# Kernel optimization log

Measured on AMD Instinct MI355X. Metric: run time of the kernel, lower is better.

## Reference

```python
import jax, jax.numpy as jnp
import numpy as np
from jax import lax

N_FFT = 1024
N_FREQ = N_FFT // 2 + 1  # 513
BATCH = 32
SAMPLES = 480000
HOP = 256


def setup_inputs() -> dict:
    key = jax.random.key(0)
    kx, kwin = jax.random.split(key)
    x = jax.random.normal(kx, (BATCH, 1, SAMPLES), dtype=jnp.float32)
    n = jnp.arange(N_FFT, dtype=jnp.float32)
    # standard rfft angular frequencies: w_k = 2*pi*k / N
    w = 2.0 * jnp.pi * jnp.arange(N_FREQ, dtype=jnp.float32) / N_FFT
    # Hann window (periodic), as typically used for STFT
    window = 0.5 - 0.5 * jnp.cos(2.0 * jnp.pi * jnp.arange(N_FFT, dtype=jnp.float32) / N_FFT)
    return {"x": x, "n": n, "w": w, "window": window, "hop_size": HOP, "power": 1}


def _create_dft_matrices(n, w, window):
    # temp[f, t] = w_f * n_t
    temp = w[:, None] * n[None, :]              # [n_freq, n_fft]
    Fr = jnp.cos(temp)
    Fi = -jnp.sin(temp)
    if window is not None:
        Fr = window * Fr
        Fi = window * Fi
    # conv1d weights: [out_ch=n_freq, in_ch=1, kernel=n_fft]
    return Fr[:, None, :], Fi[:, None, :]


def reference(x, n, w, window, hop_size, power):
    DFTr, DFTi = _create_dft_matrices(n, w, window)
    dn = ("NCH", "OIH", "NCH")
    real_x = lax.conv_general_dilated(x, DFTr, (hop_size,), "VALID", dimension_numbers=dn)
    imag_x = lax.conv_general_dilated(x, DFTi, (hop_size,), "VALID", dimension_numbers=dn)
    S = real_x ** 2 + imag_x ** 2              # [B, n_freq, n_frames]
    if not power:
        S = jnp.sqrt(S)
    return S
```

## Files before the change

kernel.cpp:

```cpp
#include <hip/hip_runtime.h>
#include <hip/hip_bf16.h>
#include <stdint.h>
#include <math.h>


#define NFFT     1024
#define NFREQ    513
#define BATCH    32
#define SAMPLES  480000
#define SAMPH    240000
#define HOPH     128
#define NFRAMES  1872
#define BN       128
#define NBPB     15
#define MBLKS    4
#define KTILES   16
#define NWG      (BATCH * NBPB * MBLKS)

#define XH_BYTES  ((size_t)BATCH * SAMPLES)
#define AWS_BYTES ((size_t)MBLKS * KTILES * 128 * 64)
#define TW_BYTES  (513 * 8)

#define XMAX   6.5f
#define SCALE_X (127.0f / XMAX)
#define DEQ    (XMAX / 16129.0f)
#define DEQ2   (DEQ * DEQ)

#define QX_BLOCKS 1875
#define BA_BLOCKS 2048
#define PREP_BLOCKS (QX_BLOCKS + BA_BLOCKS + 1)

typedef __attribute__((ext_vector_type(4)))  int i32x4;
typedef __attribute__((ext_vector_type(16))) int i32x16;

#define SLOTM(r) ((((r) >> 1) & 3) ^ (((r) >> 3) & 1))
#define SWZ(q) ((q) ^ ((((q) >> 3) ^ ((q) >> 6)) & 7))

__global__ __launch_bounds__(256) void k_prep(const float* __restrict__ x,
                                              const float* __restrict__ narr,
                                              const float* __restrict__ w,
                                              const float* __restrict__ window,
                                              signed char* __restrict__ xe,
                                              signed char* __restrict__ xo,
                                              signed char* __restrict__ Aws,
                                              float2* __restrict__ tw) {
  const int bid = blockIdx.x;
  const int tid = threadIdx.x;
  if (bid < QX_BLOCKS) {
    size_t i = (size_t)bid * 256 + tid;
    const float4* x4 = (const float4*)x;
    union { signed char c[16]; uint4 v; } pe, po;
    #pragma unroll
    for (int j = 0; j < 8; ++j) {
      float4 a = x4[i * 8 + j];
      float qe  = fminf(127.f, fmaxf(-127.f, a.x * SCALE_X));
      float qo  = fminf(127.f, fmaxf(-127.f, a.y * SCALE_X));
      float qe2 = fminf(127.f, fmaxf(-127.f, a.z * SCALE_X));
      float qo2 = fminf(127.f, fmaxf(-127.f, a.w * SCALE_X));
      pe.c[j * 2]     = (signed char)__float2int_rn(qe);
      po.c[j * 2]     = (signed char)__float2int_rn(qo);
      pe.c[j * 2 + 1] = (signed char)__float2int_rn(qe2);
      po.c[j * 2 + 1] = (signed char)__float2int_rn(qo2);
    }
    ((uint4*)xe)[i] = pe.v;
    ((uint4*)xo)[i] = po.v;
  } else if (bid < QX_BLOCKS + BA_BLOCKS) {
    uint32_t E = (uint32_t)(bid - QX_BLOCKS) * 256 + tid;
    uint32_t e    = E & 15;
    uint32_t s    = (E >> 4) & 3;
    uint32_t r    = (E >> 6) & 127;
    uint32_t kt   = (E >> 13) & 15;
    uint32_t mblk = E >> 17;
    uint32_t er = mblk * 128 + r;
    uint32_t j  = (kt & 7) * 64 + ((s ^ SLOTM(r)) << 4) + e;
    uint32_t odd = (kt >> 3) & 1;
    uint32_t widx = (er == 1) ? 512u : (er & ~1u);
    float ang = w[widx] * narr[j];
    float sn, cs;
    sincosf(ang, &sn, &cs);
    float base = ((er & 1) && (er != 1)) ? -sn : cs;
    float val = 127.f * window[2 * j + odd] * base;
    Aws[E] = (signed char)__float2int_rn(val);
  } else {
    for (int j = tid; j <= 512; j += 256) {
      float st, ct;
      sincosf((float)j * (float)(M_PI / 512.0), &st, &ct);
      tw[j] = make_float2(ct, st);
    }
  }
}

#define GL2LDS(g, l) __builtin_amdgcn_global_load_lds( \
    (const __attribute__((address_space(1))) uint32_t*)(g), \
    (__attribute__((address_space(3))) uint32_t*)(l), 16, 0, 0)

#define WAITV4_BAR() asm volatile("s_waitcnt vmcnt(4)\ns_barrier" ::: "memory")
#define WAIT0_BAR()  asm volatile("s_waitcnt vmcnt(0)\ns_barrier" ::: "memory")
#define LGKM0_BAR()  asm volatile("s_waitcnt lgkmcnt(0)\ns_barrier" ::: "memory")

#define SE 0
#define SO 17408
#define AR 34816

#define STAGE_STREAM(src, bl) do {                                              \
  _Pragma("unroll") for (int p_ = 0; p_ < 4; ++p_) {                            \
    int q_ = p_ * 256 + tid;                                                    \
    GL2LDS((src) + (SWZ(q_) << 4), &lds[(bl) + q_ * 16]);                       \
  }                                                                             \
  if (tid < 64) {                                                               \
    int q_ = 1024 + tid;                                                        \
    GL2LDS((src) + (SWZ(q_) << 4), &lds[(bl) + q_ * 16]);                       \
  }                                                                             \
} while (0)

#define STAGE_A(kt) do {                                                        \
  _Pragma("unroll") for (int j_ = 0; j_ < 2; ++j_) {                            \
    int ci_ = j_ * 256 + tid;                                                   \
    GL2LDS(Aws + (((size_t)mblk * KTILES + (kt)) * 512 + ci_) * 16,             \
           &lds[AR + ((kt) & 3) * 8192 + ci_ * 16]);                            \
  } } while (0)

#define READ_A2(dst, kt)                                                        \
  _Pragma("unroll") for (int mt_ = 0; mt_ < 2; ++mt_)                           \
  _Pragma("unroll") for (int ks_ = 0; ks_ < 2; ++ks_) {                         \
    int r_ = wr * 64 + mt_ * 32 + lr;                                           \
    int sl_ = (ks_ * 2 + hi) ^ SLOTM(r_);                                       \
    dst[mt_][ks_] = *(const i32x4*)&lds[AR + ((kt) & 3) * 8192 + (r_ * 4 + sl_) * 16]; \
  }

#define READ_B2(dst, ktm7, SB)                                                  \
  _Pragma("unroll") for (int nt_ = 0; nt_ < 2; ++nt_)                           \
  _Pragma("unroll") for (int ks_ = 0; ks_ < 2; ++ks_) {                         \
    int cp_ = (wc * 64 + nt_ * 32 + lr) * 8 + (ktm7) * 4 + 2 * ks_ + hi;        \
    dst[nt_][ks_] = *(const i32x4*)&lds[(SB) + (SWZ(cp_) << 4)];                \
  }

#define MFMA8(ACC, A_, B_) do {                                                 \
  __builtin_amdgcn_s_setprio(1);                                                \
  _Pragma("unroll") for (int ks_ = 0; ks_ < 2; ++ks_)                           \
  _Pragma("unroll") for (int mt_ = 0; mt_ < 2; ++mt_)                           \
  _Pragma("unroll") for (int nt_ = 0; nt_ < 2; ++nt_)                           \
    ACC[mt_][nt_] = __builtin_amdgcn_mfma_i32_32x32x32_i8(                      \
        A_[mt_][ks_], B_[nt_][ks_], ACC[mt_][nt_], 0, 0, 0);                    \
  __builtin_amdgcn_s_setprio(0);                                                \
  } while (0)

#define ITER(i, ACC, SB) do {                                                   \
    if ((i) == 7) WAIT0_BAR(); else WAITV4_BAR();                               \
    i32x4 a0[2][2], a1[2][2], b0[2][2], b1[2][2];                               \
    READ_A2(a0, 2 * (i));     READ_B2(b0, (2 * (i)) & 7, SB);                   \
    READ_A2(a1, 2 * (i) + 1); READ_B2(b1, (2 * (i) + 1) & 7, SB);               \
    MFMA8(ACC, a0, b0);                                                         \
    MFMA8(ACC, a1, b1);                                                         \
    LGKM0_BAR();                                                                \
    if ((i) < 6) { STAGE_A(2 * (i) + 4); STAGE_A(2 * (i) + 5); }                \
  } while (0)

__global__ __launch_bounds__(256, 2) void k_stft(const signed char* __restrict__ xe,
                                                 const signed char* __restrict__ xo,
                                                 const signed char* __restrict__ Aws,
                                                 const float2* __restrict__ tw,
                                                 float* __restrict__ out) {
  __shared__ __align__(16) signed char lds[67584];
  const int tid  = threadIdx.x;
  const int lane = tid & 63;
  const int wid  = tid >> 6;
  const int wr = wid >> 1;
  const int wc = wid & 1;
  const int lr = lane & 31;
  const int hi = lane >> 5;

  const int bx = blockIdx.x;
  const int v = (bx & 7) * 240 + (bx >> 3);
  const int mblk = v & 3;
  const int nb = v >> 2;
  const int b  = nb / NBPB;
  const int f0 = (nb - b * NBPB) * BN;

  const signed char* se_src = xe + (size_t)b * SAMPH + (size_t)f0 * HOPH;
  const signed char* so_src = xo + (size_t)b * SAMPH + (size_t)f0 * HOPH;

  i32x16 accE[2][2], accO[2][2];
  #pragma unroll
  for (int i = 0; i < 2; ++i)
    #pragma unroll
    for (int j = 0; j < 2; ++j)
      #pragma unroll
      for (int e = 0; e < 16; ++e) { accE[i][j][e] = 0; accO[i][j][e] = 0; }

  STAGE_STREAM(se_src, SE);
  STAGE_STREAM(so_src, SO);
  STAGE_A(0); STAGE_A(1); STAGE_A(2); STAGE_A(3);
  WAIT0_BAR();

  ITER(0, accE, SE); ITER(1, accE, SE); ITER(2, accE, SE); ITER(3, accE, SE);
  ITER(4, accO, SO); ITER(5, accO, SO); ITER(6, accO, SO); ITER(7, accO, SO);

  const int fbase = mblk * 64 + wr * 32;
  #pragma unroll
  for (int nt = 0; nt < 2; ++nt) {
    const int col = wc * 64 + nt * 32 + lr;
    const int tfi = f0 + col;
    if (tfi >= NFRAMES) continue;
    float* op = out + (size_t)b * ((size_t)NFREQ * NFRAMES) + tfi;
    #pragma unroll
    for (int mt = 0; mt < 2; ++mt) {
      i32x16 vE = accE[mt][nt];
      i32x16 vO = accO[mt][nt];
      #pragma unroll
      for (int aa = 0; aa < 4; ++aa)
        #pragma unroll
        for (int q = 0; q < 2; ++q) {
          const int fq = fbase + mt * 16 + aa * 4 + 2 * hi + q;
          float Ere = (float)vE[aa * 4 + 2 * q];
          float Eim = (float)vE[aa * 4 + 2 * q + 1];
          float Ore = (float)vO[aa * 4 + 2 * q];
          float Oim = (float)vO[aa * 4 + 2 * q + 1];
          if (fq == 0) {
            float sp = Ere + Ore, sm = Ere - Ore;
            op[0]                     = DEQ2 * sp * sp;
            op[(size_t)512 * NFRAMES] = DEQ2 * sm * sm;
            op[(size_t)256 * NFRAMES] = DEQ2 * (Eim * Eim + Oim * Oim);
          } else {
            float2 t = tw[fq];
            float Pre = t.x * Ore + t.y * Oim;
            float Pim = t.x * Oim - t.y * Ore;
            float ar = Ere + Pre, ai = Eim + Pim;
            float br = Ere - Pre, bi = Eim - Pim;
            op[(size_t)fq * NFRAMES]         = DEQ2 * (ar * ar + ai * ai);
            op[(size_t)(512 - fq) * NFRAMES] = DEQ2 * (br * br + bi * bi);
          }
        }
    }
  }
}

extern "C" void kernel_launch(void* const* d_in, const int* in_sizes, int n_in,
                              void* d_out, int out_size, void* d_ws, size_t ws_size,
                              hipStream_t stream) {
  const float* x      = (const float*)d_in[0];
  const float* narr   = (const float*)d_in[1];
  const float* w      = (const float*)d_in[2];
  const float* window = (const float*)d_in[3];
  float* out = (float*)d_out;

  signed char* xe  = (signed char*)d_ws;
  signed char* xo  = xe + (size_t)BATCH * SAMPH;
  signed char* Aws = xo + (size_t)BATCH * SAMPH;
  float2*      tw  = (float2*)(Aws + AWS_BYTES);
  if (ws_size < XH_BYTES + AWS_BYTES + TW_BYTES) return;

  k_prep<<<PREP_BLOCKS, 256, 0, stream>>>(x, narr, w, window, xe, xo, Aws, tw);
  k_stft<<<NWG, 256, 0, stream>>>(xe, xo, Aws, tw, out);
}
```

Before: 64.47 us.

## Loop over all frequency blocks per workgroup, reusing staged signal tile

Each workgroup now handles all four frequency blocks for one batch/frame tile in a sequential loop instead of one block per workgroup. The staged even/odd signal in LDS is reused across all four blocks, which cuts redundant global-to-LDS signal loads, and the A-matrix stream is pipelined continuously across the blocks. The frame tile shrinks to 120 with 16 tiles per batch, giving 512 workgroups instead of 1920. This lowers parallelism and tail balance, and the epilogue stores are serialized inside the loop.

Result: slower. 96.38 us (+49.5%).

```diff
diff --git a/kernel.cpp b/kernel.cpp
--- a/kernel.cpp
+++ b/kernel.cpp
@@ -11,14 +11,13 @@
 #define SAMPH    240000
 #define HOPH     128
 #define NFRAMES  1872
-#define BN       128
-#define NBPB     15
-#define MBLKS    4
-#define KTILES   16
-#define NWG      (BATCH * NBPB * MBLKS)
+#define BN       120
+#define NBPB     16
+#define NTILES   64
+#define NWG      (BATCH * NBPB)
 
 #define XH_BYTES  ((size_t)BATCH * SAMPLES)
-#define AWS_BYTES ((size_t)MBLKS * KTILES * 128 * 64)
+#define AWS_BYTES ((size_t)NTILES * 128 * 64)
 #define TW_BYTES  (513 * 8)
 
 #define XMAX   6.5f
@@ -110,22 +109,21 @@
   if (tid < 64) {                                                               \
     int q_ = 1024 + tid;                                                        \
     GL2LDS((src) + (SWZ(q_) << 4), &lds[(bl) + q_ * 16]);                       \
-  }                                                                             \
-} while (0)
-
-#define STAGE_A(kt) do {                                                        \
+  } } while (0)
+
+#define STAGE_A(t) do {                                                         \
   _Pragma("unroll") for (int j_ = 0; j_ < 2; ++j_) {                            \
     int ci_ = j_ * 256 + tid;                                                   \
-    GL2LDS(Aws + (((size_t)mblk * KTILES + (kt)) * 512 + ci_) * 16,             \
-           &lds[AR + ((kt) & 3) * 8192 + ci_ * 16]);                            \
+    GL2LDS(Aws + ((size_t)(t) * 512 + ci_) * 16,                                \
+           &lds[AR + ((t) & 3) * 8192 + ci_ * 16]);                             \
   } } while (0)
 
-#define READ_A2(dst, kt)                                                        \
+#define READ_A2(dst, t)                                                         \
   _Pragma("unroll") for (int mt_ = 0; mt_ < 2; ++mt_)                           \
   _Pragma("unroll") for (int ks_ = 0; ks_ < 2; ++ks_) {                         \
     int r_ = wr * 64 + mt_ * 32 + lr;                                           \
     int sl_ = (ks_ * 2 + hi) ^ SLOTM(r_);                                       \
-    dst[mt_][ks_] = *(const i32x4*)&lds[AR + ((kt) & 3) * 8192 + (r_ * 4 + sl_) * 16]; \
+    dst[mt_][ks_] = *(const i32x4*)&lds[AR + ((t) & 3) * 8192 + (r_ * 4 + sl_) * 16]; \
   }
 
 #define READ_B2(dst, ktm7, SB)                                                  \
@@ -145,15 +143,17 @@
   __builtin_amdgcn_s_setprio(0);                                                \
   } while (0)
 
-#define ITER(i, ACC, SB) do {                                                   \
-    if ((i) == 7) WAIT0_BAR(); else WAITV4_BAR();                               \
+#define ITER(tb, ii, ACC, SB) do {                                              \
+    const int t0_ = (tb) + 2 * (ii), t1_ = t0_ + 1;                             \
+    const int gi_ = t0_ >> 1;                                                   \
+    if (gi_ == 31) WAIT0_BAR(); else WAITV4_BAR();                              \
     i32x4 a0[2][2], a1[2][2], b0[2][2], b1[2][2];                               \
-    READ_A2(a0, 2 * (i));     READ_B2(b0, (2 * (i)) & 7, SB);                   \
-    READ_A2(a1, 2 * (i) + 1); READ_B2(b1, (2 * (i) + 1) & 7, SB);               \
+    READ_A2(a0, t0_); READ_B2(b0, t0_ & 7, SB);                                 \
+    READ_A2(a1, t1_); READ_B2(b1, t1_ & 7, SB);                                 \
     MFMA8(ACC, a0, b0);                                                         \
     MFMA8(ACC, a1, b1);                                                         \
     LGKM0_BAR();                                                                \
-    if ((i) < 6) { STAGE_A(2 * (i) + 4); STAGE_A(2 * (i) + 5); }                \
+    if (gi_ < 30) { STAGE_A(t0_ + 4); STAGE_A(t1_ + 4); }                       \
   } while (0)
 
 __global__ __launch_bounds__(256, 2) void k_stft(const signed char* __restrict__ xe,
@@ -171,11 +171,9 @@
   const int hi = lane >> 5;
 
   const int bx = blockIdx.x;
-  const int v = (bx & 7) * 240 + (bx >> 3);
-  const int mblk = v & 3;
-  const int nb = v >> 2;
-  const int b  = nb / NBPB;
-  const int f0 = (nb - b * NBPB) * BN;
+  const int nb = (bx & 7) * 64 + (bx >> 3);
+  const int b  = nb >> 4;
+  const int f0 = (nb & 15) * BN;
 
   const signed char* se_src = xe + (size_t)b * SAMPH + (size_t)f0 * HOPH;
   const signed char* so_src = xo + (size_t)b * SAMPH + (size_t)f0 * HOPH;
@@ -193,45 +191,58 @@
   STAGE_A(0); STAGE_A(1); STAGE_A(2); STAGE_A(3);
   WAIT0_BAR();
 
-  ITER(0, accE, SE); ITER(1, accE, SE); ITER(2, accE, SE); ITER(3, accE, SE);
-  ITER(4, accO, SO); ITER(5, accO, SO); ITER(6, accO, SO); ITER(7, accO, SO);
-
-  const int fbase = mblk * 64 + wr * 32;
-  #pragma unroll
-  for (int nt = 0; nt < 2; ++nt) {
-    const int col = wc * 64 + nt * 32 + lr;
-    const int tfi = f0 + col;
-    if (tfi >= NFRAMES) continue;
-    float* op = out + (size_t)b * ((size_t)NFREQ * NFRAMES) + tfi;
-    #pragma unroll
-    for (int mt = 0; mt < 2; ++mt) {
-      i32x16 vE = accE[mt][nt];
-      i32x16 vO = accO[mt][nt];
+  #pragma unroll 1
+  for (int mb = 0; mb < 4; ++mb) {
+    const int tb = mb * 16;
+    ITER(tb, 0, accE, SE); ITER(tb, 1, accE, SE);
+    ITER(tb, 2, accE, SE); ITER(tb, 3, accE, SE);
+    ITER(tb, 4, accO, SO); ITER(tb, 5, accO, SO);
+    ITER(tb, 6, accO, SO); ITER(tb, 7, accO, SO);
+
+    const int fbase = mb * 64 + wr * 32;
+    #pragma unroll
+    for (int nt = 0; nt < 2; ++nt) {
+      const int col = wc * 64 + nt * 32 + lr;
+      const int tfi = f0 + col;
+      if (tfi < NFRAMES) {
+        float* op = out + (size_t)b * ((size_t)NFREQ * NFRAMES) + tfi;
+        #pragma unroll
+        for (int mt = 0; mt < 2; ++mt) {
+          i32x16 vE = accE[mt][nt];
+          i32x16 vO = accO[mt][nt];
+          #pragma unroll
+          for (int aa = 0; aa < 4; ++aa)
+            #pragma unroll
+            for (int q = 0; q < 2; ++q) {
+              const int fq = fbase + mt * 16 + aa * 4 + 2 * hi + q;
+              float Ere = (float)vE[aa * 4 + 2 * q];
+              float Eim = (float)vE[aa * 4 + 2 * q + 1];
+              float Ore = (float)vO[aa * 4 + 2 * q];
+              float Oim = (float)vO[aa * 4 + 2 * q + 1];
+              if (fq == 0) {
+                float sp = Ere + Ore, sm = Ere - Ore;
+                op[0]                     = DEQ2 * sp * sp;
+                op[(size_t)512 * NFRAMES] = DEQ2 * sm * sm;
+                op[(size_t)256 * NFRAMES] = DEQ2 * (Eim * Eim + Oim * Oim);
+              } else {
+                float2 t = tw[fq];
+                float Pre = t.x * Ore + t.y * Oim;
+                float Pim = t.x * Oim - t.y * Ore;
+                float ar = Ere + Pre, ai = Eim + Pim;
+                float br = Ere - Pre, bi = Eim - Pim;
+                op[(size_t)fq * NFRAMES]         = DEQ2 * (ar * ar + ai * ai);
+                op[(size_t)(512 - fq) * NFRAMES] = DEQ2 * (br * br + bi * bi);
+              }
+            }
+        }
+      }
+    }
+    #pragma unroll
+    for (int i = 0; i < 2; ++i)
       #pragma unroll
-      for (int aa = 0; aa < 4; ++aa)
+      for (int j = 0; j < 2; ++j)
         #pragma unroll
-        for (int q = 0; q < 2; ++q) {
-          const int fq = fbase + mt * 16 + aa * 4 + 2 * hi + q;
-          float Ere = (float)vE[aa * 4 + 2 * q];
-          float Eim = (float)vE[aa * 4 + 2 * q + 1];
-          float Ore = (float)vO[aa * 4 + 2 * q];
-          float Oim = (float)vO[aa * 4 + 2 * q + 1];
-          if (fq == 0) {
-            float sp = Ere + Ore, sm = Ere - Ore;
-            op[0]                     = DEQ2 * sp * sp;
-            op[(size_t)512 * NFRAMES] = DEQ2 * sm * sm;
-            op[(size_t)256 * NFRAMES] = DEQ2 * (Eim * Eim + Oim * Oim);
-          } else {
-            float2 t = tw[fq];
-            float Pre = t.x * Ore + t.y * Oim;
-            float Pim = t.x * Oim - t.y * Ore;
-            float ar = Ere + Pre, ai = Eim + Pim;
-            float br = Ere - Pre, bi = Eim - Pim;
-            op[(size_t)fq * NFRAMES]         = DEQ2 * (ar * ar + ai * ai);
-            op[(size_t)(512 - fq) * NFRAMES] = DEQ2 * (br * br + bi * bi);
-          }
-        }
-    }
+        for (int e = 0; e < 16; ++e) { accE[i][j][e] = 0; accO[i][j][e] = 0; }
   }
 }
 
```

## Load DFT weight fragments directly from global memory instead of staging through LDS

Applied to the files above, without the earlier changes.

The prep kernel now writes the int8 DFT matrix in per-lane MFMA fragment order, so each wave can load its A operands straight from global memory (L2-resident) with 16-byte vector loads. This removes the LDS staging buffer for A, its barriers and wait-count pipeline, and halves the LDS footprint to 34 KB, which could allow more workgroups per CU. The cost is that A loads now go through the vector memory path, with global-load latency exposed inside a short loop and no explicit prefetch.

After: 69.20 us. 1.07x slower.

```diff
diff --git a/kernel.cpp b/kernel.cpp
--- a/kernel.cpp
+++ b/kernel.cpp
@@ -14,11 +14,10 @@
 #define BN       128
 #define NBPB     15
 #define MBLKS    4
-#define KTILES   16
 #define NWG      (BATCH * NBPB * MBLKS)
 
 #define XH_BYTES  ((size_t)BATCH * SAMPLES)
-#define AWS_BYTES ((size_t)MBLKS * KTILES * 128 * 64)
+#define AFR_BYTES ((size_t)64 * 8192)
 #define TW_BYTES  (513 * 8)
 
 #define XMAX   6.5f
@@ -33,7 +32,6 @@
 typedef __attribute__((ext_vector_type(4)))  int i32x4;
 typedef __attribute__((ext_vector_type(16))) int i32x16;
 
-#define SLOTM(r) ((((r) >> 1) & 3) ^ (((r) >> 3) & 1))
 #define SWZ(q) ((q) ^ ((((q) >> 3) ^ ((q) >> 6)) & 7))
 
 __global__ __launch_bounds__(256) void k_prep(const float* __restrict__ x,
@@ -42,7 +40,7 @@
                                               const float* __restrict__ window,
                                               signed char* __restrict__ xe,
                                               signed char* __restrict__ xo,
-                                              signed char* __restrict__ Aws,
+                                              signed char* __restrict__ Afr,
                                               float2* __restrict__ tw) {
   const int bid = blockIdx.x;
   const int tid = threadIdx.x;
@@ -67,20 +65,23 @@
   } else if (bid < QX_BLOCKS + BA_BLOCKS) {
     uint32_t E = (uint32_t)(bid - QX_BLOCKS) * 256 + tid;
     uint32_t e    = E & 15;
-    uint32_t s    = (E >> 4) & 3;
-    uint32_t r    = (E >> 6) & 127;
-    uint32_t kt   = (E >> 13) & 15;
-    uint32_t mblk = E >> 17;
-    uint32_t er = mblk * 128 + r;
-    uint32_t j  = (kt & 7) * 64 + ((s ^ SLOTM(r)) << 4) + e;
-    uint32_t odd = (kt >> 3) & 1;
-    uint32_t widx = (er == 1) ? 512u : (er & ~1u);
+    uint32_t lane = (E >> 4) & 63;
+    uint32_t ks   = (E >> 10) & 1;
+    uint32_t mt   = (E >> 11) & 1;
+    uint32_t wr   = (E >> 12) & 1;
+    uint32_t t    = E >> 13;
+    uint32_t kt   = t & 15;
+    uint32_t mblk = t >> 4;
+    uint32_t hi   = lane >> 5;
+    uint32_t gr   = mblk * 128 + wr * 64 + mt * 32 + (lane & 31);
+    uint32_t j    = (kt & 7) * 64 + (2 * ks + hi) * 16 + e;
+    uint32_t odd  = (kt >> 3) & 1;
+    uint32_t widx = (gr == 1) ? 512u : (gr & ~1u);
     float ang = w[widx] * narr[j];
     float sn, cs;
     sincosf(ang, &sn, &cs);
-    float base = ((er & 1) && (er != 1)) ? -sn : cs;
-    float val = 127.f * window[2 * j + odd] * base;
-    Aws[E] = (signed char)__float2int_rn(val);
+    float base = ((gr & 1) && (gr != 1)) ? -sn : cs;
+    Afr[E] = (signed char)__float2int_rn(127.f * window[2 * j + odd] * base);
   } else {
     for (int j = tid; j <= 512; j += 256) {
       float st, ct;
@@ -94,13 +95,10 @@
     (const __attribute__((address_space(1))) uint32_t*)(g), \
     (__attribute__((address_space(3))) uint32_t*)(l), 16, 0, 0)
 
-#define WAITV4_BAR() asm volatile("s_waitcnt vmcnt(4)\ns_barrier" ::: "memory")
 #define WAIT0_BAR()  asm volatile("s_waitcnt vmcnt(0)\ns_barrier" ::: "memory")
-#define LGKM0_BAR()  asm volatile("s_waitcnt lgkmcnt(0)\ns_barrier" ::: "memory")
 
 #define SE 0
 #define SO 17408
-#define AR 34816
 
 #define STAGE_STREAM(src, bl) do {                                              \
   _Pragma("unroll") for (int p_ = 0; p_ < 4; ++p_) {                            \
@@ -110,23 +108,13 @@
   if (tid < 64) {                                                               \
     int q_ = 1024 + tid;                                                        \
     GL2LDS((src) + (SWZ(q_) << 4), &lds[(bl) + q_ * 16]);                       \
-  }                                                                             \
-} while (0)
-
-#define STAGE_A(kt) do {                                                        \
-  _Pragma("unroll") for (int j_ = 0; j_ < 2; ++j_) {                            \
-    int ci_ = j_ * 256 + tid;                                                   \
-    GL2LDS(Aws + (((size_t)mblk * KTILES + (kt)) * 512 + ci_) * 16,             \
-           &lds[AR + ((kt) & 3) * 8192 + ci_ * 16]);                            \
   } } while (0)
 
-#define READ_A2(dst, kt)                                                        \
+#define LOAD_A(dst, kt)                                                         \
   _Pragma("unroll") for (int mt_ = 0; mt_ < 2; ++mt_)                           \
-  _Pragma("unroll") for (int ks_ = 0; ks_ < 2; ++ks_) {                         \
-    int r_ = wr * 64 + mt_ * 32 + lr;                                           \
-    int sl_ = (ks_ * 2 + hi) ^ SLOTM(r_);                                       \
-    dst[mt_][ks_] = *(const i32x4*)&lds[AR + ((kt) & 3) * 8192 + (r_ * 4 + sl_) * 16]; \
-  }
+  _Pragma("unroll") for (int ks_ = 0; ks_ < 2; ++ks_)                           \
+    dst[mt_][ks_] = *(const i32x4*)(Ablk + (size_t)(kt) * 8192 +                \
+                                    mt_ * 2048 + ks_ * 1024);
 
 #define READ_B2(dst, ktm7, SB)                                                  \
   _Pragma("unroll") for (int nt_ = 0; nt_ < 2; ++nt_)                           \
@@ -145,23 +133,19 @@
   __builtin_amdgcn_s_setprio(0);                                                \
   } while (0)
 
-#define ITER(i, ACC, SB) do {                                                   \
-    if ((i) == 7) WAIT0_BAR(); else WAITV4_BAR();                               \
-    i32x4 a0[2][2], a1[2][2], b0[2][2], b1[2][2];                               \
-    READ_A2(a0, 2 * (i));     READ_B2(b0, (2 * (i)) & 7, SB);                   \
-    READ_A2(a1, 2 * (i) + 1); READ_B2(b1, (2 * (i) + 1) & 7, SB);               \
-    MFMA8(ACC, a0, b0);                                                         \
-    MFMA8(ACC, a1, b1);                                                         \
-    LGKM0_BAR();                                                                \
-    if ((i) < 6) { STAGE_A(2 * (i) + 4); STAGE_A(2 * (i) + 5); }                \
+#define KT(kt, ACC, SB) do {                                                    \
+    i32x4 af[2][2], bf[2][2];                                                   \
+    LOAD_A(af, kt);                                                             \
+    READ_B2(bf, (kt) & 7, SB);                                                  \
+    MFMA8(ACC, af, bf);                                                         \
   } while (0)
 
 __global__ __launch_bounds__(256, 2) void k_stft(const signed char* __restrict__ xe,
                                                  const signed char* __restrict__ xo,
-                                                 const signed char* __restrict__ Aws,
+                                                 const signed char* __restrict__ Afr,
                                                  const float2* __restrict__ tw,
                                                  float* __restrict__ out) {
-  __shared__ __align__(16) signed char lds[67584];
+  __shared__ __align__(16) signed char lds[34816];
   const int tid  = threadIdx.x;
   const int lane = tid & 63;
   const int wid  = tid >> 6;
@@ -179,6 +163,8 @@
 
   const signed char* se_src = xe + (size_t)b * SAMPH + (size_t)f0 * HOPH;
   const signed char* so_src = xo + (size_t)b * SAMPH + (size_t)f0 * HOPH;
+  const signed char* Ablk = Afr + (size_t)mblk * 16 * 8192 +
+                            wr * 4096 + lane * 16;
 
   i32x16 accE[2][2], accO[2][2];
   #pragma unroll
@@ -190,11 +176,12 @@
 
   STAGE_STREAM(se_src, SE);
   STAGE_STREAM(so_src, SO);
-  STAGE_A(0); STAGE_A(1); STAGE_A(2); STAGE_A(3);
   WAIT0_BAR();
 
-  ITER(0, accE, SE); ITER(1, accE, SE); ITER(2, accE, SE); ITER(3, accE, SE);
-  ITER(4, accO, SO); ITER(5, accO, SO); ITER(6, accO, SO); ITER(7, accO, SO);
+  #pragma unroll 2
+  for (int kt = 0; kt < 8; ++kt)  KT(kt, accE, SE);
+  #pragma unroll 2
+  for (int kt = 8; kt < 16; ++kt) KT(kt, accO, SO);
 
   const int fbase = mblk * 64 + wr * 32;
   #pragma unroll
@@ -246,10 +233,10 @@
 
   signed char* xe  = (signed char*)d_ws;
   signed char* xo  = xe + (size_t)BATCH * SAMPH;
-  signed char* Aws = xo + (size_t)BATCH * SAMPH;
-  float2*      tw  = (float2*)(Aws + AWS_BYTES);
-  if (ws_size < XH_BYTES + AWS_BYTES + TW_BYTES) return;
-
-  k_prep<<<PREP_BLOCKS, 256, 0, stream>>>(x, narr, w, window, xe, xo, Aws, tw);
-  k_stft<<<NWG, 256, 0, stream>>>(xe, xo, Aws, tw, out);
+  signed char* Afr = xo + (size_t)BATCH * SAMPH;
+  float2*      tw  = (float2*)(Afr + AFR_BYTES);
+  if (ws_size < XH_BYTES + AFR_BYTES + TW_BYTES) return;
+
+  k_prep<<<PREP_BLOCKS, 256, 0, stream>>>(x, narr, w, window, xe, xo, Afr, tw);
+  k_stft<<<NWG, 256, 0, stream>>>(xe, xo, Afr, tw, out);
 }
```
